# Performance work log

Measured on AMD Instinct MI355X. Metric: run time of the kernel, lower is better.

Reference implementation:

```python
import jax, jax.numpy as jnp
import numpy as np
from jax import lax

T, IN, H, OUT = 4096, 1024, 2048, 512


def setup_inputs() -> dict:
    key = jax.random.key(0)
    ks = jax.random.split(key, 11)
    s = 1.0 / np.sqrt(IN + H)
    s2 = 1.0 / np.sqrt(2 * H)
    def lin(k, o, i, sc):
        kw, kb = jax.random.split(k)
        W = jax.random.uniform(kw, (o, i), minval=-sc, maxval=sc, dtype=jnp.float32)
        b = jax.random.uniform(kb, (o,), minval=-sc, maxval=sc, dtype=jnp.float32)
        return W, b
    Wi, bi = lin(ks[0], H, IN + H, s)
    Wf, bf = lin(ks[1], H, IN + H, s)
    Wo, bo = lin(ks[2], H, IN + H, s)
    Wc, bc = lin(ks[3], H, IN + H, s)
    W2, b2 = lin(ks[4], OUT, 2 * H, s2)
    x = jax.random.normal(ks[5], (T, IN), dtype=jnp.float32)
    return {"input": x, "Wi": Wi, "bi": bi, "Wf": Wf, "bf": bf,
            "Wo": Wo, "bo": bo, "Wc": Wc, "bc": bc, "W2": W2, "b2": b2}


def reference(input, Wi, bi, Wf, bf, Wo, bo, Wc, bc, W2, b2):
    n_in = input.shape[1]
    # split each gate weight into input part and hidden part (cat(x, h) layout)
    def split(W):
        return W[:, :n_in], W[:, n_in:]
    Wix, Wih = split(Wi); Wfx, Wfh = split(Wf)
    Wox, Woh = split(Wo); Wcx, Wch = split(Wc)
    # precompute the input contribution for all timesteps in one GEMM each
    xi = input @ Wix.T + bi  # [T, H]
    xf = input @ Wfx.T + bf
    xo = input @ Wox.T + bo
    xc = input @ Wcx.T + bc

    def step(carry, xs):
        h, c = carry
        xi_t, xf_t, xo_t, xc_t = xs
        i = jax.nn.sigmoid(xi_t + Wih @ h)
        f = jax.nn.sigmoid(xf_t + Wfh @ h)
        o = jax.nn.sigmoid(xo_t + Woh @ h)
        c_tilde = jnp.tanh(xc_t + Wch @ h)
        c = f * c + i * c_tilde
        h = o * jnp.tanh(c)
        return (h, c), None

    h0 = jnp.zeros((Wih.shape[0],), dtype=input.dtype)
    c0 = jnp.zeros_like(h0)
    (h, c), _ = lax.scan(step, (h0, c0), (xi, xf, xo, xc))
    output = W2 @ jnp.concatenate([h, c]) + b2
    return output, h
```

## Files before the change

kernel.cpp:

```cpp
#include <hip/hip_runtime.h>
#include <stdint.h>

#define T_STEPS 4096
#define IN_DIM  1024
#define H_DIM   2048
#define OUT_DIM 512
#define W_STRIDE 3072
#define NBLK    256
#define NTHR    512
#define POLL_GUARD 65536

typedef __attribute__((ext_vector_type(4))) float floatx4;

__device__ __forceinline__ int swz(int q) { return q ^ ((q >> 3) & 7); }

__device__ __forceinline__ float fsigmoid(float v) {
  return __builtin_amdgcn_rcpf(1.f + __expf(-v));
}
__device__ __forceinline__ float ftanh(float v) {
  return 1.f - 2.f * __builtin_amdgcn_rcpf(1.f + __expf(2.f * v));
}
__device__ __forceinline__ unsigned umin2(unsigned a, unsigned b) {
  return a < b ? a : b;
}

#define WDECL(r) floatx4 w##r##_0, w##r##_1, w##r##_2, w##r##_3, w##r##_4, w##r##_5
#define WLOAD(r) do { const float* rp_ = wbase + (size_t)(r) * W_STRIDE;      \
    w##r##_0 = *(const floatx4*)(rp_ +  0);                                   \
    w##r##_1 = *(const floatx4*)(rp_ +  4);                                   \
    w##r##_2 = *(const floatx4*)(rp_ +  8);                                   \
    w##r##_3 = *(const floatx4*)(rp_ + 12);                                   \
    w##r##_4 = *(const floatx4*)(rp_ + 16);                                   \
    w##r##_5 = *(const floatx4*)(rp_ + 20); } while (0)
#define WPIN(r) asm volatile("" : "+v"(w##r##_0), "+v"(w##r##_1),             \
    "+v"(w##r##_2), "+v"(w##r##_3), "+v"(w##r##_4), "+v"(w##r##_5))
#define FMA4(acc, wq) do {                                                    \
    acc = fmaf(wq.x, v.x, acc); acc = fmaf(wq.y, v.y, acc);                   \
    acc = fmaf(wq.z, v.z, acc); acc = fmaf(wq.w, v.w, acc); } while (0)
#define FMAJ(j) do { v = *(const floatx4*)(xh + a_v##j);                      \
    FMA4(ac0, w0_##j); FMA4(ac1, w1_##j); FMA4(ac2, w2_##j);                  \
    FMA4(ac3, w3_##j); FMA4(ac4, w4_##j); FMA4(ac5, w5_##j);                  \
    FMA4(ac6, w6_##j); FMA4(ac7, w7_##j); } while (0)
#define WRED(acc, r) do { float a_ = acc;                                     \
    a_ += __shfl_down(a_, 32, 64); a_ += __shfl_down(a_, 16, 64);             \
    a_ += __shfl_down(a_, 8, 64);  a_ += __shfl_down(a_, 4, 64);              \
    a_ += __shfl_down(a_, 2, 64);  a_ += __shfl_down(a_, 1, 64);              \
    if (lane == 0) red[wv * 8 + (r)] = a_; } while (0)

__global__ __launch_bounds__(NTHR, 2)
void lstm_scan(const float* __restrict__ Wi, const float* __restrict__ Wf,
               const float* __restrict__ Wo, const float* __restrict__ Wc,
               const float* __restrict__ bi, const float* __restrict__ bff,
               const float* __restrict__ bo, const float* __restrict__ bc,
               const float* __restrict__ x,
               unsigned long long* __restrict__ hcomm,
               float* __restrict__ hbuf,
               float* __restrict__ cbuf)
{
  __shared__ float xh[768 * 4];
  __shared__ float red[8 * 8];
  __shared__ float bl[32];
  __shared__ float cl[8];

  const int tid  = threadIdx.x;
  const int b    = blockIdx.x;
  const int row0 = b << 3;
  const int grp  = tid >> 7;
  const int u    = tid & 127;
  const int wv   = tid >> 6;
  const int lane = tid & 63;

  const float* Wsel = (grp == 0) ? Wi : (grp == 1) ? Wf : (grp == 2) ? Wo : Wc;
  const float* wbase = Wsel + (size_t)row0 * W_STRIDE + 24 * u;

  WDECL(0); WDECL(1); WDECL(2); WDECL(3);
  WDECL(4); WDECL(5); WDECL(6); WDECL(7);
  WLOAD(0); WLOAD(1); WLOAD(2); WLOAD(3);
  WLOAD(4); WLOAD(5); WLOAD(6); WLOAD(7);
  WPIN(0); WPIN(1); WPIN(2); WPIN(3);
  WPIN(4); WPIN(5); WPIN(6); WPIN(7);

  if (tid < 32) {
    const float* Bsel = (tid < 8) ? bi : (tid < 16) ? bff : (tid < 24) ? bo : bc;
    bl[tid] = Bsel[row0 + (tid & 7)];
  }
  if (tid < 8) cl[tid] = 0.f;
  __syncthreads();

  const int a_v0 = swz(6 * u + 0) << 2;
  const int a_v1 = swz(6 * u + 1) << 2;
  const int a_v2 = swz(6 * u + 2) << 2;
  const int a_v3 = swz(6 * u + 3) << 2;
  const int a_v4 = swz(6 * u + 4) << 2;
  const int a_v5 = swz(6 * u + 5) << 2;
  const int hw0 = (swz(256 + (tid >> 2) +   0) << 2) + (tid & 3);
  const int hw1 = (swz(256 + (tid >> 2) + 128) << 2) + (tid & 3);
  const int hw2 = (swz(256 + (tid >> 2) + 256) << 2) + (tid & 3);
  const int hw3 = (swz(256 + (tid >> 2) + 384) << 2) + (tid & 3);

  float hlast = 0.f;
  int   alive = 1;

  for (int t = 0; t < T_STEPS; ++t) {
    if (tid >= 256) {
      const int q = tid - 256;
      const floatx4 xv = *(const floatx4*)(x + ((size_t)t << 10) + (q << 2));
      *(floatx4*)(xh + (swz(q) << 2)) = xv;
    }

    {
      unsigned long long* hb = hcomm + ((size_t)(t & 1) << 11);
      const unsigned tt = (unsigned)t;
      unsigned long long p0 = 0, p1 = 0, p2 = 0, p3 = 0;
      int guard = 0;
      while (alive) {
        p0 = __hip_atomic_load(&hb[tid], __ATOMIC_RELAXED,
                               __HIP_MEMORY_SCOPE_AGENT);
        p1 = __hip_atomic_load(&hb[tid + 512], __ATOMIC_RELAXED,
                               __HIP_MEMORY_SCOPE_AGENT);
        p2 = __hip_atomic_load(&hb[tid + 1024], __ATOMIC_RELAXED,
                               __HIP_MEMORY_SCOPE_AGENT);
        p3 = __hip_atomic_load(&hb[tid + 1536], __ATOMIC_RELAXED,
                               __HIP_MEMORY_SCOPE_AGENT);
        const unsigned mn = umin2(umin2((unsigned)(p0 >> 32),
                                        (unsigned)(p1 >> 32)),
                                  umin2((unsigned)(p2 >> 32),
                                        (unsigned)(p3 >> 32)));
        if (mn >= tt) break;
        if (++guard > POLL_GUARD) { alive = 0; break; }
        __builtin_amdgcn_s_sleep(1);
      }
      xh[hw0] = __uint_as_float((unsigned)p0);
      xh[hw1] = __uint_as_float((unsigned)p1);
      xh[hw2] = __uint_as_float((unsigned)p2);
      xh[hw3] = __uint_as_float((unsigned)p3);
    }
    __syncthreads();

    float ac0 = 0.f, ac1 = 0.f, ac2 = 0.f, ac3 = 0.f,
          ac4 = 0.f, ac5 = 0.f, ac6 = 0.f, ac7 = 0.f;
    {
      floatx4 v;
      FMAJ(0); FMAJ(1); FMAJ(2); FMAJ(3); FMAJ(4); FMAJ(5);
    }

    WRED(ac0, 0); WRED(ac1, 1); WRED(ac2, 2); WRED(ac3, 3);
    WRED(ac4, 4); WRED(ac5, 5); WRED(ac6, 6); WRED(ac7, 7);
    __syncthreads();

    if (tid < 8) {
      const int rr = tid;
      const float pi = bl[rr]      + red[0 * 8 + rr] + red[1 * 8 + rr];
      const float pf = bl[8 + rr]  + red[2 * 8 + rr] + red[3 * 8 + rr];
      const float po = bl[16 + rr] + red[4 * 8 + rr] + red[5 * 8 + rr];
      const float pc = bl[24 + rr] + red[6 * 8 + rr] + red[7 * 8 + rr];
      const float iv = fsigmoid(pi);
      const float fv = fsigmoid(pf);
      const float ov = fsigmoid(po);
      const float ct = ftanh(pc);
      const float cn = fv * cl[rr] + iv * ct;
      cl[rr] = cn;
      const float hv = ov * ftanh(cn);
      hlast = hv;
      const unsigned long long pk =
          ((unsigned long long)(unsigned)(t + 1) << 32) |
          (unsigned long long)__float_as_uint(hv);
      __hip_atomic_store(&hcomm[(((size_t)((t + 1) & 1)) << 11) + row0 + rr],
                         pk, __ATOMIC_RELAXED, __HIP_MEMORY_SCOPE_AGENT);
    }
  }

  if (tid < 8) {
    hbuf[row0 + tid] = hlast;
    cbuf[row0 + tid] = cl[tid];
  }
}

__global__ __launch_bounds__(256)
void final_kernel(const float* __restrict__ W2, const float* __restrict__ b2,
                  const float* __restrict__ hfin, const float* __restrict__ cfin,
                  float* __restrict__ out)
{
  const int wv   = threadIdx.x >> 6;
  const int lane = threadIdx.x & 63;
  const int row  = (blockIdx.x << 2) + wv;
  const float* wr = W2 + (size_t)row * (2 * H_DIM);
  float acc = 0.f;
#pragma unroll 4
  for (int k = lane; k < H_DIM; k += 64) {
    acc = fmaf(wr[k], hfin[k], acc);
    acc = fmaf(wr[H_DIM + k], cfin[k], acc);
  }
#pragma unroll
  for (int off = 32; off > 0; off >>= 1) acc += __shfl_down(acc, off, 64);
  if (lane == 0) out[row] = acc + b2[row];
}

__global__ __launch_bounds__(256)
void copy_h_kernel(const float* __restrict__ hfin, float* __restrict__ out)
{
  const int i = blockIdx.x * 256 + threadIdx.x;
  if (i < H_DIM) out[OUT_DIM + i] = hfin[i];
}

extern "C" void kernel_launch(void* const* d_in, const int* in_sizes, int n_in,
                              void* d_out, int out_size, void* d_ws, size_t ws_size,
                              hipStream_t stream)
{
  const float* x   = (const float*)d_in[0];
  const float* Wi  = (const float*)d_in[1];
  const float* bi  = (const float*)d_in[2];
  const float* Wf  = (const float*)d_in[3];
  const float* bff = (const float*)d_in[4];
  const float* Wo  = (const float*)d_in[5];
  const float* bo  = (const float*)d_in[6];
  const float* Wc  = (const float*)d_in[7];
  const float* bc  = (const float*)d_in[8];
  const float* W2  = (const float*)d_in[9];
  const float* b2  = (const float*)d_in[10];
  float* out = (float*)d_out;

  char* ws = (char*)d_ws;
  unsigned long long* hcomm = (unsigned long long*)ws;
  float* hbuf = (float*)(ws + 2 * H_DIM * sizeof(unsigned long long));
  float* cbuf = hbuf + H_DIM;

  hipMemsetAsync(hcomm, 0, 2 * H_DIM * sizeof(unsigned long long), stream);

  lstm_scan<<<dim3(NBLK), dim3(NTHR), 0, stream>>>(
      Wi, Wf, Wo, Wc, bi, bff, bo, bc, x, hcomm, hbuf, cbuf);
  final_kernel<<<dim3(OUT_DIM / 4), 256, 0, stream>>>(W2, b2, hbuf, cbuf, out);
  copy_h_kernel<<<dim3((H_DIM + 255) / 256), 256, 0, stream>>>(hbuf, out);
}
```

Baseline: 16.72 ms.

## Overlap input-projection FMAs with the hidden-state poll, splitting x and h weight slices

Each thread now holds separate register slices for the input part (8 columns) and the hidden part (16 columns) of its weight rows. It loads x_t directly from global into registers and computes the input contribution before and while waiting for h_{t-1} to be published. The first poll is issued speculatively before those FMAs, which takes the x work off the critical path after synchronisation. Shared memory shrinks to hold only h, and the shared-memory staging of x is removed. In exchange, every thread reads x from global each step instead of a shared copy.

```diff
diff --git a/kernel.cpp b/kernel.cpp
--- a/kernel.cpp
+++ b/kernel.cpp
@@ -24,23 +24,30 @@
   return a < b ? a : b;
 }
 
-#define WDECL(r) floatx4 w##r##_0, w##r##_1, w##r##_2, w##r##_3, w##r##_4, w##r##_5
-#define WLOAD(r) do { const float* rp_ = wbase + (size_t)(r) * W_STRIDE;      \
-    w##r##_0 = *(const floatx4*)(rp_ +  0);                                   \
-    w##r##_1 = *(const floatx4*)(rp_ +  4);                                   \
-    w##r##_2 = *(const floatx4*)(rp_ +  8);                                   \
-    w##r##_3 = *(const floatx4*)(rp_ + 12);                                   \
-    w##r##_4 = *(const floatx4*)(rp_ + 16);                                   \
-    w##r##_5 = *(const floatx4*)(rp_ + 20); } while (0)
-#define WPIN(r) asm volatile("" : "+v"(w##r##_0), "+v"(w##r##_1),             \
-    "+v"(w##r##_2), "+v"(w##r##_3), "+v"(w##r##_4), "+v"(w##r##_5))
-#define FMA4(acc, wq) do {                                                    \
+#define FMA4(acc, wq, v) do {                                                 \
     acc = fmaf(wq.x, v.x, acc); acc = fmaf(wq.y, v.y, acc);                   \
     acc = fmaf(wq.z, v.z, acc); acc = fmaf(wq.w, v.w, acc); } while (0)
-#define FMAJ(j) do { v = *(const floatx4*)(xh + a_v##j);                      \
-    FMA4(ac0, w0_##j); FMA4(ac1, w1_##j); FMA4(ac2, w2_##j);                  \
-    FMA4(ac3, w3_##j); FMA4(ac4, w4_##j); FMA4(ac5, w5_##j);                  \
-    FMA4(ac6, w6_##j); FMA4(ac7, w7_##j); } while (0)
+#define WDECL(r) floatx4 wx##r##_0, wx##r##_1,                                \
+    wh##r##_0, wh##r##_1, wh##r##_2, wh##r##_3
+#define WLOAD(r) do {                                                         \
+    const float* rx_ = wxb + (size_t)(r) * W_STRIDE;                          \
+    const float* rh_ = whb + (size_t)(r) * W_STRIDE;                          \
+    wx##r##_0 = *(const floatx4*)(rx_ + 0);                                   \
+    wx##r##_1 = *(const floatx4*)(rx_ + 4);                                   \
+    wh##r##_0 = *(const floatx4*)(rh_ + 0);                                   \
+    wh##r##_1 = *(const floatx4*)(rh_ + 4);                                   \
+    wh##r##_2 = *(const floatx4*)(rh_ + 8);                                   \
+    wh##r##_3 = *(const floatx4*)(rh_ + 12); } while (0)
+#define WPIN(r) asm volatile("" : "+v"(wx##r##_0), "+v"(wx##r##_1),           \
+    "+v"(wh##r##_0), "+v"(wh##r##_1), "+v"(wh##r##_2), "+v"(wh##r##_3))
+#define XFMA(r) do { FMA4(ac##r, wx##r##_0, xa);                              \
+    FMA4(ac##r, wx##r##_1, xb); } while (0)
+#define HFMAK(k) do {                                                         \
+    const floatx4 v = *(const floatx4*)(hl + a_h##k);                         \
+    FMA4(ac0, wh0_##k, v); FMA4(ac1, wh1_##k, v);                             \
+    FMA4(ac2, wh2_##k, v); FMA4(ac3, wh3_##k, v);                             \
+    FMA4(ac4, wh4_##k, v); FMA4(ac5, wh5_##k, v);                             \
+    FMA4(ac6, wh6_##k, v); FMA4(ac7, wh7_##k, v); } while (0)
 #define WRED(acc, r) do { float a_ = acc;                                     \
     a_ += __shfl_down(a_, 32, 64); a_ += __shfl_down(a_, 16, 64);             \
     a_ += __shfl_down(a_, 8, 64);  a_ += __shfl_down(a_, 4, 64);              \
@@ -57,7 +64,7 @@
                float* __restrict__ hbuf,
                float* __restrict__ cbuf)
 {
-  __shared__ float xh[768 * 4];
+  __shared__ float hl[512 * 4];
   __shared__ float red[8 * 8];
   __shared__ float bl[32];
   __shared__ float cl[8];
@@ -71,7 +78,8 @@
   const int lane = tid & 63;
 
   const float* Wsel = (grp == 0) ? Wi : (grp == 1) ? Wf : (grp == 2) ? Wo : Wc;
-  const float* wbase = Wsel + (size_t)row0 * W_STRIDE + 24 * u;
+  const float* wxb = Wsel + (size_t)row0 * W_STRIDE + (u << 3);
+  const float* whb = Wsel + (size_t)row0 * W_STRIDE + IN_DIM + (u << 4);
 
   WDECL(0); WDECL(1); WDECL(2); WDECL(3);
   WDECL(4); WDECL(5); WDECL(6); WDECL(7);
@@ -87,62 +95,66 @@
   if (tid < 8) cl[tid] = 0.f;
   __syncthreads();
 
-  const int a_v0 = swz(6 * u + 0) << 2;
-  const int a_v1 = swz(6 * u + 1) << 2;
-  const int a_v2 = swz(6 * u + 2) << 2;
-  const int a_v3 = swz(6 * u + 3) << 2;
-  const int a_v4 = swz(6 * u + 4) << 2;
-  const int a_v5 = swz(6 * u + 5) << 2;
-  const int hw0 = (swz(256 + (tid >> 2) +   0) << 2) + (tid & 3);
-  const int hw1 = (swz(256 + (tid >> 2) + 128) << 2) + (tid & 3);
-  const int hw2 = (swz(256 + (tid >> 2) + 256) << 2) + (tid & 3);
-  const int hw3 = (swz(256 + (tid >> 2) + 384) << 2) + (tid & 3);
+  const int a_h0 = swz(4 * u + 0) << 2;
+  const int a_h1 = swz(4 * u + 1) << 2;
+  const int a_h2 = swz(4 * u + 2) << 2;
+  const int a_h3 = swz(4 * u + 3) << 2;
+  const int hv0 = (swz((tid >> 2) +   0) << 2) + (tid & 3);
+  const int hv1 = (swz((tid >> 2) + 128) << 2) + (tid & 3);
+  const int hv2 = (swz((tid >> 2) + 256) << 2) + (tid & 3);
+  const int hv3 = (swz((tid >> 2) + 384) << 2) + (tid & 3);
 
   float hlast = 0.f;
   int   alive = 1;
 
   for (int t = 0; t < T_STEPS; ++t) {
-    if (tid >= 256) {
-      const int q = tid - 256;
-      const floatx4 xv = *(const floatx4*)(x + ((size_t)t << 10) + (q << 2));
-      *(floatx4*)(xh + (swz(q) << 2)) = xv;
-    }
+    const float* xp = x + ((size_t)t << 10) + (u << 3);
+    const floatx4 xa = *(const floatx4*)(xp);
+    const floatx4 xb = *(const floatx4*)(xp + 4);
+
+    unsigned long long* hb = hcomm + ((size_t)(t & 1) << 11);
+    const unsigned tt = (unsigned)t;
+    unsigned long long p0, p1, p2, p3;
+    p0 = __hip_atomic_load(&hb[tid], __ATOMIC_RELAXED,
+                           __HIP_MEMORY_SCOPE_AGENT);
+    p1 = __hip_atomic_load(&hb[tid + 512], __ATOMIC_RELAXED,
+                           __HIP_MEMORY_SCOPE_AGENT);
+    p2 = __hip_atomic_load(&hb[tid + 1024], __ATOMIC_RELAXED,
+                           __HIP_MEMORY_SCOPE_AGENT);
+    p3 = __hip_atomic_load(&hb[tid + 1536], __ATOMIC_RELAXED,
+                           __HIP_MEMORY_SCOPE_AGENT);
+
+    float ac0 = 0.f, ac1 = 0.f, ac2 = 0.f, ac3 = 0.f,
+          ac4 = 0.f, ac5 = 0.f, ac6 = 0.f, ac7 = 0.f;
+    XFMA(0); XFMA(1); XFMA(2); XFMA(3);
+    XFMA(4); XFMA(5); XFMA(6); XFMA(7);
 
     {
-      unsigned long long* hb = hcomm + ((size_t)(t & 1) << 11);
-      const unsigned tt = (unsigned)t;
-      unsigned long long p0 = 0, p1 = 0, p2 = 0, p3 = 0;
+      unsigned mn = umin2(umin2((unsigned)(p0 >> 32), (unsigned)(p1 >> 32)),
+                          umin2((unsigned)(p2 >> 32), (unsigned)(p3 >> 32)));
       int guard = 0;
-      while (alive) {
-        p0 = __hip_atomic_load(&hb[tid], __ATOMIC_RELAXED,
-                               __HIP_MEMORY_SCOPE_AGENT);
-        p1 = __hip_atomic_load(&hb[tid + 512], __ATOMIC_RELAXED,
-                               __HIP_MEMORY_SCOPE_AGENT);
-        p2 = __hip_atomic_load(&hb[tid + 1024], __ATOMIC_RELAXED,
-                               __HIP_MEMORY_SCOPE_AGENT);
-        p3 = __hip_atomic_load(&hb[tid + 1536], __ATOMIC_RELAXED,
-                               __HIP_MEMORY_SCOPE_AGENT);
-        const unsigned mn = umin2(umin2((unsigned)(p0 >> 32),
-                                        (unsigned)(p1 >> 32)),
-                                  umin2((unsigned)(p2 >> 32),
-                                        (unsigned)(p3 >> 32)));
-        if (mn >= tt) break;
+      while (alive && mn < tt) {
         if (++guard > POLL_GUARD) { alive = 0; break; }
         __builtin_amdgcn_s_sleep(1);
+        p0 = __hip_atomic_load(&hb[tid], __ATOMIC_RELAXED,
+                               __HIP_MEMORY_SCOPE_AGENT);
+        p1 = __hip_atomic_load(&hb[tid + 512], __ATOMIC_RELAXED,
+                               __HIP_MEMORY_SCOPE_AGENT);
+        p2 = __hip_atomic_load(&hb[tid + 1024], __ATOMIC_RELAXED,
+                               __HIP_MEMORY_SCOPE_AGENT);
+        p3 = __hip_atomic_load(&hb[tid + 1536], __ATOMIC_RELAXED,
+                               __HIP_MEMORY_SCOPE_AGENT);
+        mn = umin2(umin2((unsigned)(p0 >> 32), (unsigned)(p1 >> 32)),
+                   umin2((unsigned)(p2 >> 32), (unsigned)(p3 >> 32)));
       }
-      xh[hw0] = __uint_as_float((unsigned)p0);
-      xh[hw1] = __uint_as_float((unsigned)p1);
-      xh[hw2] = __uint_as_float((unsigned)p2);
-      xh[hw3] = __uint_as_float((unsigned)p3);
     }
+    hl[hv0] = __uint_as_float((unsigned)p0);
+    hl[hv1] = __uint_as_float((unsigned)p1);
+    hl[hv2] = __uint_as_float((unsigned)p2);
+    hl[hv3] = __uint_as_float((unsigned)p3);
     __syncthreads();
 
-    float ac0 = 0.f, ac1 = 0.f, ac2 = 0.f, ac3 = 0.f,
-          ac4 = 0.f, ac5 = 0.f, ac6 = 0.f, ac7 = 0.f;
-    {
-      floatx4 v;
-      FMAJ(0); FMAJ(1); FMAJ(2); FMAJ(3); FMAJ(4); FMAJ(5);
-    }
+    HFMAK(0); HFMAK(1); HFMAK(2); HFMAK(3);
 
     WRED(ac0, 0); WRED(ac1, 1); WRED(ac2, 2); WRED(ac3, 3);
     WRED(ac4, 4); WRED(ac5, 5); WRED(ac6, 6); WRED(ac7, 7);
```

After: 16.62 ms. Within noise of the previous version (-0.6%).
